# Kernel tuning notes

Hardware: AMD Instinct MI355X
Metric: run time of the kernel (lower is better)

Reference implementation:

```python
import jax, jax.numpy as jnp
import numpy as np

REGIONS = [(0, 16), (17, 21), (22, 26), (27, 30), (31, 35), (36, 41), (42, 47), (48, 59), (60, 67)]
LN_EPS = 1e-5


def setup_inputs() -> dict:
    key = jax.random.key(0)
    ks = jax.random.split(key, 8)
    B, T, N, D = 32, 128, 68, 128
    sc = 1.0 / np.sqrt(D)
    inp = {
        "lm_data": jax.random.normal(ks[0], (B, T, N, D), jnp.float32),
        "adj": jax.random.uniform(ks[1], (77, 77), jnp.float32) / 77.0,
        "Wr": jax.random.normal(ks[2], (D, 1), jnp.float32) * sc,
        "br": jnp.zeros((1,), jnp.float32),
        "W0": jax.random.normal(ks[3], (D, D), jnp.float32) * sc,
        "b0": jnp.zeros((D,), jnp.float32),
        "W1": jax.random.normal(ks[4], (D, D), jnp.float32) * sc,
        "b1": jnp.zeros((D,), jnp.float32),
        "W2": jax.random.normal(ks[5], (D, D), jnp.float32) * sc,
        "b2": jnp.zeros((D,), jnp.float32),
        "W3": jax.random.normal(ks[6], (D, D), jnp.float32) * sc,
        "b3": jnp.zeros((D,), jnp.float32),
        "gamma": jnp.ones((D,), jnp.float32),
        "beta": jnp.zeros((D,), jnp.float32),
    }
    return inp


def _region_pool(x, Wr, br):
    # x: [B,T,R,D] -> attention-pooled [B,T,D]
    scores = jnp.einsum('btrd,do->btro', x, Wr) + br  # [B,T,R,1]
    w = jax.nn.softmax(scores, axis=-2)
    return jnp.sum(w * x, axis=-2)


def reference(lm_data, adj, Wr, br, W0, b0, W1, b1, W2, b2, W3, b3, gamma, beta):
    # init_global_nodes: gather each region, attention-pool, scatter into 9 global nodes
    global_nodes = jnp.stack(
        [_region_pool(lm_data[..., s:e + 1, :], Wr, br) for s, e in REGIONS], axis=2
    )  # [B,T,9,D]
    x = jnp.concatenate([lm_data, global_nodes], axis=2)  # [B,T,77,D]

    # 4-layer residual GCN: relu(Linear(adj @ x))
    layers = [(W0, b0), (W1, b1), (W2, b2), (W3, b3)]
    residual = x
    for i, (W, b) in enumerate(layers):
        agg = jnp.einsum('nm,btmd->btnd', adj, x)
        out = jax.nn.relu(agg @ W + b)
        if i < len(layers) - 1:
            out = out + residual  # feature dims all equal
            residual = out
        x = out

    # LayerNorm (dropout is identity at eval)
    mu = jnp.mean(x, axis=-1, keepdims=True)
    var = jnp.var(x, axis=-1, keepdims=True)
    x = (x - mu) / jnp.sqrt(var + LN_EPS) * gamma + beta
    return x
```

## Files before the change

### kernel.cpp

```cpp
#include <hip/hip_runtime.h>
#include <stdint.h>

typedef __attribute__((ext_vector_type(8))) short bf16x8;
typedef __attribute__((ext_vector_type(4))) float f32x4;
typedef unsigned short u16;
typedef __attribute__((ext_vector_type(4))) unsigned short us4;
typedef __attribute__((ext_vector_type(8))) unsigned short us8;

#define NP 104
#define FPD 136

__device__ __constant__ int c_RS[9] = {0, 17, 22, 27, 31, 36, 42, 48, 60};
__device__ __constant__ int c_RE[9] = {16, 21, 26, 30, 35, 41, 47, 59, 67};

__device__ __forceinline__ float b2f(u16 h) {
    union { unsigned int u; float f; } v;
    v.u = ((unsigned int)h) << 16;
    return v.f;
}
__device__ __forceinline__ u16 f2b(float f) {
    union { float f; unsigned int u; } v;
    v.f = f;
    unsigned int r = v.u + 0x7fffu + ((v.u >> 16) & 1u);
    return (u16)(r >> 16);
}

__global__ void prep_kernel(const float* __restrict__ adj,
                            const float* __restrict__ W0, const float* __restrict__ W1,
                            const float* __restrict__ W2, const float* __restrict__ W3,
                            u16* __restrict__ adjp, u16* __restrict__ WT) {
    int id = blockIdx.x * 256 + threadIdx.x;
    if (id < 80 * 96) {
        int m = id / 96, k = id - m * 96;
        adjp[id] = (m < 77 && k < 77) ? f2b(adj[m * 77 + k]) : (u16)0;
    }
    {
        int l = id >> 14, r = id & 16383;
        int n = r >> 7, k = r & 127;
        const float* W = (l == 0) ? W0 : (l == 1) ? W1 : (l == 2) ? W2 : W3;
        WT[id] = f2b(W[k * 128 + n]);
    }
}

__global__ __launch_bounds__(256, 2) void gcn_kernel(
    const float* __restrict__ lm, const float* __restrict__ Wr,
    const float* __restrict__ b0, const float* __restrict__ b1,
    const float* __restrict__ b2, const float* __restrict__ b3,
    const float* __restrict__ gamma, const float* __restrict__ beta,
    const u16* __restrict__ adjp, const u16* __restrict__ WT,
    float* __restrict__ out) {
    __shared__ __align__(16) u16 xT[128 * NP];
    __shared__ __align__(16) u16 ag[80 * FPD];
    __shared__ float WrF[128];
    __shared__ float biasF[512];
    __shared__ float gamF[128], betF[128];
    __shared__ float scoreS[80], wtS[80], muS[80], rsS[80];

    const int t = threadIdx.x;
    const int lane = t & 63;
    const int w = t >> 6;
    const int lo = lane & 15;
    const int qd = lane >> 4;
    const size_t pos = blockIdx.x;
    const float* lmp = lm + pos * (68 * 128);

    if (t < 128) {
        WrF[t] = Wr[t];
        gamF[t] = gamma[t];
        betF[t] = beta[t];
        biasF[t] = b0[t];
        biasF[128 + t] = b1[t];
        biasF[256 + t] = b2[t];
        biasF[384 + t] = b3[t];
    }
    for (int i = t; i < 128 * NP / 8; i += 256) ((uint4*)xT)[i] = make_uint4(0, 0, 0, 0);
    const float4* lmp4 = (const float4*)lmp;
    for (int c = t; c < 68 * 32; c += 256) {
        int n = c >> 5, q = c & 31;
        float4 v = lmp4[c];
        us4 o;
        o[0] = f2b(v.x); o[1] = f2b(v.y); o[2] = f2b(v.z); o[3] = f2b(v.w);
        *(us4*)(&ag[n * FPD + q * 4]) = o;
    }
    __syncthreads();

    for (int c = t; c < 68 * 16; c += 256) {
        int d8 = c / 68, n = c - d8 * 68;
        us8 v = *(const us8*)(&ag[n * FPD + d8 * 8]);
#pragma unroll
        for (int j = 0; j < 8; j++) xT[(d8 * 8 + j) * NP + n] = v[j];
    }
    if (t < 68) {
        float s = 0.f;
        for (int d8 = 0; d8 < 16; d8++) {
            us8 v = *(const us8*)(&ag[t * FPD + d8 * 8]);
#pragma unroll
            for (int j = 0; j < 8; j++) s += b2f(v[j]) * WrF[d8 * 8 + j];
        }
        scoreS[t] = s;
    }
    __syncthreads();

    if (t < 9) {
        int s0 = c_RS[t], e0 = c_RE[t];
        float mx = -3e38f;
        for (int i = s0; i <= e0; i++) mx = fmaxf(mx, scoreS[i]);
        float sum = 0.f;
        for (int i = s0; i <= e0; i++) sum += __expf(scoreS[i] - mx);
        float inv = 1.f / sum;
        for (int i = s0; i <= e0; i++) wtS[i] = __expf(scoreS[i] - mx) * inv;
    }
    __syncthreads();

    for (int c = t; c < 9 * 128; c += 256) {
        int r = c >> 7, d = c & 127;
        int s0 = c_RS[r], e0 = c_RE[r];
        float g = 0.f;
        for (int n = s0; n <= e0; n++) g += wtS[n] * b2f(ag[n * FPD + d]);
        xT[d * NP + 68 + r] = f2b(g);
    }
    __syncthreads();

    for (int l = 0; l < 4; l++) {
        f32x4 acc[5][2];
#pragma unroll
        for (int a = 0; a < 5; a++)
#pragma unroll
            for (int j = 0; j < 2; j++)
#pragma unroll
                for (int r = 0; r < 4; r++) acc[a][j][r] = 0.f;
#pragma unroll
        for (int ks = 0; ks < 3; ks++) {
            bf16x8 bA[5], bB[2];
#pragma unroll
            for (int tm = 0; tm < 5; tm++)
                bA[tm] = *(const bf16x8*)(adjp + (tm * 16 + lo) * 96 + ks * 32 + qd * 8);
#pragma unroll
            for (int j = 0; j < 2; j++) {
                int tn = w + 4 * j;
                bB[j] = *(const bf16x8*)(&xT[(tn * 16 + lo) * NP + ks * 32 + qd * 8]);
            }
#pragma unroll
            for (int tm = 0; tm < 5; tm++)
#pragma unroll
                for (int j = 0; j < 2; j++)
                    acc[tm][j] = __builtin_amdgcn_mfma_f32_16x16x32_bf16(bA[tm], bB[j], acc[tm][j], 0, 0, 0);
        }
#pragma unroll
        for (int tm = 0; tm < 5; tm++)
#pragma unroll
            for (int j = 0; j < 2; j++) {
                int col = (w + 4 * j) * 16 + lo;
#pragma unroll
                for (int r = 0; r < 4; r++) {
                    int row = tm * 16 + qd * 4 + r;
                    ag[row * FPD + col] = f2b(acc[tm][j][r]);
                }
            }
        __syncthreads();

#pragma unroll
        for (int a = 0; a < 5; a++)
#pragma unroll
            for (int j = 0; j < 2; j++)
#pragma unroll
                for (int r = 0; r < 4; r++) acc[a][j][r] = 0.f;
        const u16* WTl = WT + l * 16384;
#pragma unroll
        for (int ks = 0; ks < 4; ks++) {
            bf16x8 aF[5], bW[2];
#pragma unroll
            for (int tm = 0; tm < 5; tm++)
                aF[tm] = *(const bf16x8*)(&ag[(tm * 16 + lo) * FPD + ks * 32 + qd * 8]);
#pragma unroll
            for (int j = 0; j < 2; j++) {
                int tn = w + 4 * j;
                bW[j] = *(const bf16x8*)(WTl + (tn * 16 + lo) * 128 + ks * 32 + qd * 8);
            }
#pragma unroll
            for (int tm = 0; tm < 5; tm++)
#pragma unroll
                for (int j = 0; j < 2; j++)
                    acc[tm][j] = __builtin_amdgcn_mfma_f32_16x16x32_bf16(aF[tm], bW[j], acc[tm][j], 0, 0, 0);
        }
        if (l == 3) __syncthreads();
#pragma unroll
        for (int j = 0; j < 2; j++) {
            int col = (w + 4 * j) * 16 + lo;
            float bv = biasF[l * 128 + col];
#pragma unroll
            for (int tm = 0; tm < 5; tm++)
#pragma unroll
                for (int r = 0; r < 4; r++) {
                    int row = tm * 16 + qd * 4 + r;
                    float v = fmaxf(acc[tm][j][r] + bv, 0.f);
                    if (l < 3) {
                        v += b2f(xT[col * NP + row]);
                        xT[col * NP + row] = f2b(v);
                    } else {
                        ag[row * FPD + col] = f2b(v);
                    }
                }
        }
        __syncthreads();
    }

    if (t < 77) {
        float s = 0.f, ss = 0.f;
        for (int d = 0; d < 128; d += 2) {
            uint32_t v = *(const uint32_t*)(&ag[t * FPD + d]);
            float a = b2f((u16)(v & 0xffff)), b = b2f((u16)(v >> 16));
            s += a + b;
            ss += a * a + b * b;
        }
        float mu = s * (1.f / 128.f);
        float var = ss * (1.f / 128.f) - mu * mu;
        muS[t] = mu;
        rsS[t] = rsqrtf(var + 1e-5f);
    }
    __syncthreads();

    float* outp = out + pos * 9856;
    for (int c = t; c < 77 * 32; c += 256) {
        int n = c >> 5, q = c & 31;
        us4 v = *(const us4*)(&ag[n * FPD + q * 4]);
        float mu = muS[n], rs = rsS[n];
        float4 o;
        int d = q * 4;
        o.x = (b2f(v[0]) - mu) * rs * gamF[d + 0] + betF[d + 0];
        o.y = (b2f(v[1]) - mu) * rs * gamF[d + 1] + betF[d + 1];
        o.z = (b2f(v[2]) - mu) * rs * gamF[d + 2] + betF[d + 2];
        o.w = (b2f(v[3]) - mu) * rs * gamF[d + 3] + betF[d + 3];
        *(float4*)(outp + n * 128 + d) = o;
    }
}

extern "C" void kernel_launch(void* const* d_in, const int* in_sizes, int n_in,
                              void* d_out, int out_size, void* d_ws, size_t ws_size,
                              hipStream_t stream) {
    const float* lm = (const float*)d_in[0];
    const float* adj = (const float*)d_in[1];
    const float* Wr = (const float*)d_in[2];
    const float* W0 = (const float*)d_in[4];
    const float* b0 = (const float*)d_in[5];
    const float* W1 = (const float*)d_in[6];
    const float* b1 = (const float*)d_in[7];
    const float* W2 = (const float*)d_in[8];
    const float* b2 = (const float*)d_in[9];
    const float* W3 = (const float*)d_in[10];
    const float* b3 = (const float*)d_in[11];
    const float* gamma = (const float*)d_in[12];
    const float* beta = (const float*)d_in[13];

    u16* adjp = (u16*)d_ws;
    u16* WT = (u16*)((char*)d_ws + 80 * 96 * 2);

    prep_kernel<<<256, 256, 0, stream>>>(adj, W0, W1, W2, W3, adjp, WT);
    gcn_kernel<<<4096, 256, 0, stream>>>(lm, Wr, b0, b1, b2, b3, gamma, beta,
                                         adjp, WT, (float*)d_out);
}
```

Before: 507.6 us.

## Use 512 threads per block with one 16-column tile per wave and shuffle softmax

The kernel goes from 4 to 8 waves per block, so each wave owns a single 16-wide feature tile, and the launch-bounds occupancy hint rises. The aggregation MFMA swaps operands (xT as A, adj as B) so results can be written back as packed 4-element vectors instead of scalar LDS stores. The residual update now also uses vector loads and stores. Region softmax runs as a warp-shuffle reduction across 288 threads rather than 9 serial threads, and the global load is reordered ahead of the xT zeroing. The risks are higher register pressure from the aggressive launch bounds and more adj/weight global traffic per wave.

```diff
diff --git a/kernel.cpp b/kernel.cpp
--- a/kernel.cpp
+++ b/kernel.cpp
@@ -42,7 +42,7 @@
     }
 }
 
-__global__ __launch_bounds__(256, 2) void gcn_kernel(
+__global__ __launch_bounds__(512, 6) void gcn_kernel(
     const float* __restrict__ lm, const float* __restrict__ Wr,
     const float* __restrict__ b0, const float* __restrict__ b1,
     const float* __restrict__ b2, const float* __restrict__ b3,
@@ -62,8 +62,15 @@
     const int lo = lane & 15;
     const int qd = lane >> 4;
     const size_t pos = blockIdx.x;
-    const float* lmp = lm + pos * (68 * 128);
-
+
+    const float4* lmp4 = (const float4*)(lm + pos * (68 * 128));
+    for (int c = t; c < 68 * 32; c += 512) {
+        int n = c >> 5, q = c & 31;
+        float4 v = lmp4[c];
+        us4 o;
+        o[0] = f2b(v.x); o[1] = f2b(v.y); o[2] = f2b(v.z); o[3] = f2b(v.w);
+        *(us4*)(&ag[n * FPD + q * 4]) = o;
+    }
     if (t < 128) {
         WrF[t] = Wr[t];
         gamF[t] = gamma[t];
@@ -73,18 +80,10 @@
         biasF[256 + t] = b2[t];
         biasF[384 + t] = b3[t];
     }
-    for (int i = t; i < 128 * NP / 8; i += 256) ((uint4*)xT)[i] = make_uint4(0, 0, 0, 0);
-    const float4* lmp4 = (const float4*)lmp;
-    for (int c = t; c < 68 * 32; c += 256) {
-        int n = c >> 5, q = c & 31;
-        float4 v = lmp4[c];
-        us4 o;
-        o[0] = f2b(v.x); o[1] = f2b(v.y); o[2] = f2b(v.z); o[3] = f2b(v.w);
-        *(us4*)(&ag[n * FPD + q * 4]) = o;
-    }
-    __syncthreads();
-
-    for (int c = t; c < 68 * 16; c += 256) {
+    for (int i = t; i < 128 * NP / 8; i += 512) ((uint4*)xT)[i] = make_uint4(0, 0, 0, 0);
+    __syncthreads();
+
+    for (int c = t; c < 68 * 16; c += 512) {
         int d8 = c / 68, n = c - d8 * 68;
         us8 v = *(const us8*)(&ag[n * FPD + d8 * 8]);
 #pragma unroll
@@ -101,18 +100,22 @@
     }
     __syncthreads();
 
-    if (t < 9) {
-        int s0 = c_RS[t], e0 = c_RE[t];
-        float mx = -3e38f;
-        for (int i = s0; i <= e0; i++) mx = fmaxf(mx, scoreS[i]);
-        float sum = 0.f;
-        for (int i = s0; i <= e0; i++) sum += __expf(scoreS[i] - mx);
-        float inv = 1.f / sum;
-        for (int i = s0; i <= e0; i++) wtS[i] = __expf(scoreS[i] - mx) * inv;
-    }
-    __syncthreads();
-
-    for (int c = t; c < 9 * 128; c += 256) {
+    if (t < 288) {
+        int r = t >> 5, i = t & 31;
+        int s0 = c_RS[r], len = c_RE[r] - s0 + 1;
+        float s = (i < len) ? scoreS[s0 + i] : -3e38f;
+        float m = s;
+#pragma unroll
+        for (int d = 1; d < 32; d <<= 1) m = fmaxf(m, __shfl_xor(m, d, 64));
+        float e = (i < len) ? __expf(s - m) : 0.f;
+        float sum = e;
+#pragma unroll
+        for (int d = 1; d < 32; d <<= 1) sum += __shfl_xor(sum, d, 64);
+        if (i < len) wtS[s0 + i] = e / sum;
+    }
+    __syncthreads();
+
+    for (int c = t; c < 9 * 128; c += 512) {
         int r = c >> 7, d = c & 127;
         int s0 = c_RS[r], e0 = c_RE[r];
         float g = 0.f;
@@ -122,84 +125,68 @@
     __syncthreads();
 
     for (int l = 0; l < 4; l++) {
-        f32x4 acc[5][2];
+        f32x4 acc[5];
 #pragma unroll
         for (int a = 0; a < 5; a++)
 #pragma unroll
-            for (int j = 0; j < 2; j++)
-#pragma unroll
-                for (int r = 0; r < 4; r++) acc[a][j][r] = 0.f;
+            for (int r = 0; r < 4; r++) acc[a][r] = 0.f;
+
 #pragma unroll
         for (int ks = 0; ks < 3; ks++) {
-            bf16x8 bA[5], bB[2];
+            bf16x8 aA = *(const bf16x8*)(&xT[(w * 16 + lo) * NP + ks * 32 + qd * 8]);
+            bf16x8 bB[5];
+#pragma unroll
+            for (int tn = 0; tn < 5; tn++)
+                bB[tn] = *(const bf16x8*)(adjp + (tn * 16 + lo) * 96 + ks * 32 + qd * 8);
+#pragma unroll
+            for (int tn = 0; tn < 5; tn++)
+                acc[tn] = __builtin_amdgcn_mfma_f32_16x16x32_bf16(aA, bB[tn], acc[tn], 0, 0, 0);
+        }
+#pragma unroll
+        for (int tn = 0; tn < 5; tn++) {
+            us4 o;
+#pragma unroll
+            for (int r = 0; r < 4; r++) o[r] = f2b(acc[tn][r]);
+            *(us4*)(&ag[(tn * 16 + lo) * FPD + w * 16 + qd * 4]) = o;
+        }
+        __syncthreads();
+
+#pragma unroll
+        for (int a = 0; a < 5; a++)
+#pragma unroll
+            for (int r = 0; r < 4; r++) acc[a][r] = 0.f;
+        const u16* WTl = WT + l * 16384;
+#pragma unroll
+        for (int ks = 0; ks < 4; ks++) {
+            bf16x8 bW = *(const bf16x8*)(WTl + (w * 16 + lo) * 128 + ks * 32 + qd * 8);
+            bf16x8 aF[5];
 #pragma unroll
             for (int tm = 0; tm < 5; tm++)
-                bA[tm] = *(const bf16x8*)(adjp + (tm * 16 + lo) * 96 + ks * 32 + qd * 8);
-#pragma unroll
-            for (int j = 0; j < 2; j++) {
-                int tn = w + 4 * j;
-                bB[j] = *(const bf16x8*)(&xT[(tn * 16 + lo) * NP + ks * 32 + qd * 8]);
+                aF[tm] = *(const bf16x8*)(&ag[(tm * 16 + lo) * FPD + ks * 32 + qd * 8]);
+#pragma unroll
+            for (int tm = 0; tm < 5; tm++)
+                acc[tm] = __builtin_amdgcn_mfma_f32_16x16x32_bf16(aF[tm], bW, acc[tm], 0, 0, 0);
+        }
+        if (l == 3) __syncthreads();
+        float bv = biasF[l * 128 + w * 16 + lo];
+        if (l < 3) {
+#pragma unroll
+            for (int tm = 0; tm < 5; tm++) {
+                int a = (w * 16 + lo) * NP + tm * 16 + qd * 4;
+                us4 old = *(const us4*)(&xT[a]);
+                us4 o;
+#pragma unroll
+                for (int r = 0; r < 4; r++)
+                    o[r] = f2b(fmaxf(acc[tm][r] + bv, 0.f) + b2f(old[r]));
+                *(us4*)(&xT[a]) = o;
             }
+        } else {
 #pragma unroll
             for (int tm = 0; tm < 5; tm++)
-#pragma unroll
-                for (int j = 0; j < 2; j++)
-                    acc[tm][j] = __builtin_amdgcn_mfma_f32_16x16x32_bf16(bA[tm], bB[j], acc[tm][j], 0, 0, 0);
-        }
-#pragma unroll
-        for (int tm = 0; tm < 5; tm++)
-#pragma unroll
-            for (int j = 0; j < 2; j++) {
-                int col = (w + 4 * j) * 16 + lo;
 #pragma unroll
                 for (int r = 0; r < 4; r++) {
                     int row = tm * 16 + qd * 4 + r;
-                    ag[row * FPD + col] = f2b(acc[tm][j][r]);
-                }
-            }
-        __syncthreads();
-
-#pragma unroll
-        for (int a = 0; a < 5; a++)
-#pragma unroll
-            for (int j = 0; j < 2; j++)
-#pragma unroll
-                for (int r = 0; r < 4; r++) acc[a][j][r] = 0.f;
-        const u16* WTl = WT + l * 16384;
-#pragma unroll
-        for (int ks = 0; ks < 4; ks++) {
-            bf16x8 aF[5], bW[2];
-#pragma unroll
-            for (int tm = 0; tm < 5; tm++)
-                aF[tm] = *(const bf16x8*)(&ag[(tm * 16 + lo) * FPD + ks * 32 + qd * 8]);
-#pragma unroll
-            for (int j = 0; j < 2; j++) {
-                int tn = w + 4 * j;
-                bW[j] = *(const bf16x8*)(WTl + (tn * 16 + lo) * 128 + ks * 32 + qd * 8);
-            }
-#pragma unroll
-            for (int tm = 0; tm < 5; tm++)
-#pragma unroll
-                for (int j = 0; j < 2; j++)
-                    acc[tm][j] = __builtin_amdgcn_mfma_f32_16x16x32_bf16(aF[tm], bW[j], acc[tm][j], 0, 0, 0);
-        }
-        if (l == 3) __syncthreads();
-#pragma unroll
-        for (int j = 0; j < 2; j++) {
-            int col = (w + 4 * j) * 16 + lo;
-            float bv = biasF[l * 128 + col];
-#pragma unroll
-            for (int tm = 0; tm < 5; tm++)
-#pragma unroll
-                for (int r = 0; r < 4; r++) {
-                    int row = tm * 16 + qd * 4 + r;
-                    float v = fmaxf(acc[tm][j][r] + bv, 0.f);
-                    if (l < 3) {
-                        v += b2f(xT[col * NP + row]);
-                        xT[col * NP + row] = f2b(v);
-                    } else {
-                        ag[row * FPD + col] = f2b(v);
-                    }
+                    ag[row * FPD + w * 16 + lo] = f2b(fmaxf(acc[tm][r] + bv, 0.f));
                 }
         }
         __syncthreads();
@@ -221,7 +208,7 @@
     __syncthreads();
 
     float* outp = out + pos * 9856;
-    for (int c = t; c < 77 * 32; c += 256) {
+    for (int c = t; c < 77 * 32; c += 512) {
         int n = c >> 5, q = c & 31;
         us4 v = *(const us4*)(&ag[n * FPD + q * 4]);
         float mu = muS[n], rs = rsS[n];
@@ -256,6 +243,6 @@
     u16* WT = (u16*)((char*)d_ws + 80 * 96 * 2);
 
     prep_kernel<<<256, 256, 0, stream>>>(adj, W0, W1, W2, W3, adjp, WT);
-    gcn_kernel<<<4096, 256, 0, stream>>>(lm, Wr, b0, b1, b2, b3, gamma, beta,
+    gcn_kernel<<<4096, 512, 0, stream>>>(lm, Wr, b0, b1, b2, b3, gamma, beta,
                                          adjp, WT, (float*)d_out);
 }
```

Result: slower. 564.0 us (+11.1%).
